# Kernel optimization log

Hardware: AMD Instinct MI355X
Metric: run time of the kernel (lower is better)

Reference implementation:

```python
import jax, jax.numpy as jnp
import numpy as np

N, D, IN_DIM, H, L = 20000, 32, 3, 64, 3


def _lstm_agg(h_nodes, nbr_sorted, W_ih, W_hh, b_ih, b_hh):
    """Batched LSTM over each node's (sorted) neighbor sequence; returns final hidden state h_T."""
    n = h_nodes.shape[0]
    hidden = W_hh.shape[1]

    def step(carry, idx):
        h, c = carry
        x = h_nodes[idx]                                     # [N, in_d] irregular gather
        gates = x @ W_ih.T + h @ W_hh.T + b_ih + b_hh        # [N, 4H], torch gate order i,f,g,o
        i_g, f_g, g_g, o_g = jnp.split(gates, 4, axis=-1)
        c = jax.nn.sigmoid(f_g) * c + jax.nn.sigmoid(i_g) * jnp.tanh(g_g)
        h = jax.nn.sigmoid(o_g) * jnp.tanh(c)
        return (h, c), None

    init = (jnp.zeros((n, hidden), h_nodes.dtype), jnp.zeros((n, hidden), h_nodes.dtype))
    (h_T, _), _ = jax.lax.scan(step, init, nbr_sorted.T)      # scan over D neighbor slots
    return h_T


def _layer(h, nbr_sorted, W_ih, W_hh, b_ih, b_hh, Wl, bl):
    agg = _lstm_agg(h, nbr_sorted, W_ih, W_hh, b_ih, b_hh)    # [N, H]
    comb = jnp.concatenate([h, agg], axis=-1)                 # [N, in_d + H]
    return jax.nn.relu(comb @ Wl.T + bl)


def _forward(node_features, nbr, params, W_out, b_out):
    nbr_sorted = jnp.sort(nbr, axis=1)   # permutation-invariant ordering (Eq. 9)
    h = node_features
    for p in params:
        h = _layer(h, nbr_sorted, *p)
    return (h @ W_out.T + b_out).squeeze(-1)   # [N] per-node log-likelihood scores


def setup_inputs():
    key = jax.random.key(0)
    ks = jax.random.split(key, 40)
    inp = {}
    inp["node_features"] = jax.random.normal(ks[0], (N, IN_DIM), jnp.float32)
    inp["nbr"] = jax.random.randint(ks[1], (N, D), 0, N, jnp.int32)
    k = 2
    s = 1.0 / np.sqrt(H)
    for l in range(L):
        in_d = IN_DIM if l == 0 else H
        inp[f"W_ih{l}"] = (jax.random.normal(ks[k], (4 * H, in_d)) * (1.0 / np.sqrt(in_d))).astype(jnp.float32); k += 1
        inp[f"W_hh{l}"] = (jax.random.normal(ks[k], (4 * H, H)) * s).astype(jnp.float32); k += 1
        inp[f"b_ih{l}"] = (jax.random.normal(ks[k], (4 * H,)) * s).astype(jnp.float32); k += 1
        inp[f"b_hh{l}"] = (jax.random.normal(ks[k], (4 * H,)) * s).astype(jnp.float32); k += 1
        inp[f"Wl{l}"] = (jax.random.normal(ks[k], (H, in_d + H)) * (1.0 / np.sqrt(in_d + H))).astype(jnp.float32); k += 1
        inp[f"bl{l}"] = (jax.random.normal(ks[k], (H,)) * s).astype(jnp.float32); k += 1
    inp["W_out"] = (jax.random.normal(ks[k], (1, H)) * s).astype(jnp.float32); k += 1
    inp["b_out"] = jnp.zeros((1,), jnp.float32)
    return inp


def reference(node_features, nbr, W_ih0, W_hh0, b_ih0, b_hh0, Wl0, bl0, W_ih1, W_hh1, b_ih1, b_hh1, Wl1, bl1, W_ih2, W_hh2, b_ih2, b_hh2, Wl2, bl2, W_out, b_out):
    params = [
        (W_ih0, W_hh0, b_ih0, b_hh0, Wl0, bl0),
        (W_ih1, W_hh1, b_ih1, b_hh1, Wl1, bl1),
        (W_ih2, W_hh2, b_ih2, b_hh2, Wl2, bl2),
    ]
    return _forward(node_features, nbr, params, W_out, b_out)
```

## Files before the change

kernel.cpp:

```cpp
#include <hip/hip_runtime.h>
#include <hip/hip_bf16.h>

#define NN 20000
#define NG 1250
#define LOG2E 1.44269504088896f
#define TWOLOG2E 2.88539008177793f

typedef __attribute__((ext_vector_type(8))) short short8;
typedef __attribute__((ext_vector_type(4))) float floatx4;

__device__ __forceinline__ floatx4 MF(short8 a, short8 b, floatx4 c) {
    return __builtin_amdgcn_mfma_f32_16x16x32_bf16(a, b, c, 0, 0, 0);
}
__device__ __forceinline__ float ex2(float x) { return __builtin_amdgcn_exp2f(x); }
__device__ __forceinline__ float rcp(float x) { return __builtin_amdgcn_rcpf(x); }
__device__ __forceinline__ float clamp30(float x) {
    return __builtin_fminf(__builtin_fmaxf(x, -30.f), 30.f);
}
__device__ __forceinline__ unsigned short bf16r(float x) {
    return __builtin_bit_cast(unsigned short, __float2bfloat16(x));
}
__device__ __forceinline__ void lds_barrier() {
    asm volatile("s_waitcnt lgkmcnt(0)\n\ts_barrier" ::: "memory");
}
__device__ __forceinline__ int rowswz(int L) {
    return L ^ (((L >> 4) & 1) << 1) ^ ((L >> 3) & 1);
}

#define PREP_TOT (40960 + 49152 + 12288 + 12288 + 768 + 640000)
__global__ void prep_kernel(const float* __restrict__ x, const int* __restrict__ nbr,
    const float* __restrict__ Wih0, const float* __restrict__ Whh0,
    const float* __restrict__ bih0, const float* __restrict__ bhh0, const float* __restrict__ Wl0,
    const float* __restrict__ Wih1, const float* __restrict__ Whh1,
    const float* __restrict__ bih1, const float* __restrict__ bhh1, const float* __restrict__ Wl1,
    const float* __restrict__ Wih2, const float* __restrict__ Whh2,
    const float* __restrict__ bih2, const float* __restrict__ bhh2, const float* __restrict__ Wl2,
    unsigned short* __restrict__ Wih_p, unsigned short* __restrict__ Whh_p,
    unsigned short* __restrict__ Wlx_p, unsigned short* __restrict__ Wlh_p,
    float* __restrict__ bsum, unsigned short* __restrict__ x32, int* __restrict__ nbrT)
{
    int tid = blockIdx.x * 256 + threadIdx.x;
    if (tid < NN) {
        int v[32];
        const int4* src = (const int4*)(nbr + tid * 32);
        #pragma unroll
        for (int i = 0; i < 8; i++) {
            int4 t = src[i];
            v[4*i] = t.x; v[4*i+1] = t.y; v[4*i+2] = t.z; v[4*i+3] = t.w;
        }
        #pragma unroll
        for (int k = 2; k <= 32; k <<= 1)
            #pragma unroll
            for (int j = k >> 1; j > 0; j >>= 1)
                #pragma unroll
                for (int i = 0; i < 32; i++) {
                    int ixj = i ^ j;
                    if (ixj > i) {
                        bool up = (i & k) == 0;
                        int a = v[i], b = v[ixj];
                        bool sw = up ? (a > b) : (a < b);
                        if (sw) { v[i] = b; v[ixj] = a; }
                    }
                }
        int g = tid >> 4, m = tid & 15;
        int base = g * 512 + m;
        #pragma unroll
        for (int t = 0; t < 32; t++) nbrT[base + t * 16] = v[t];
    }
    for (int i = blockIdx.x * 256 + threadIdx.x; i < PREP_TOT; i += gridDim.x * 256) {
        int j = i;
        if (j < 40960) {
            if (j < 8192) {
                int jL = j & 7, lane = (j >> 3) & 63, t = (j >> 9) & 7, w = (j >> 12) & 1;
                int col = 64*(t>>1) + 32*w + 16*(t&1) + (lane & 15);
                int k   = (lane >> 4)*8 + jL;
                float sc = ((t>>1) == 2) ? TWOLOG2E : LOG2E;
                Wih_p[j] = bf16r((k < 3) ? Wih0[col*3 + k] * sc : 0.f);
            } else {
                int jj = j - 8192; int l = (jj >> 14) + 1; jj &= 16383;
                int jL = jj & 7, lane = (jj >> 3) & 63, kc = (jj >> 9) & 1;
                int t = (jj >> 10) & 7, w = (jj >> 13) & 1;
                int col = 64*(t>>1) + 32*w + 16*(t&1) + (lane & 15);
                int k   = kc*32 + (lane >> 4)*8 + jL;
                const float* W = (l == 1) ? Wih1 : Wih2;
                float sc = ((t>>1) == 2) ? TWOLOG2E : LOG2E;
                Wih_p[j] = bf16r(W[col*64 + k] * sc);
            }
            continue;
        }
        j -= 40960;
        if (j < 49152) {
            int l = j >> 14, e = j & 16383;
            int col = e >> 6, k = e & 63;
            const float* W = (l == 0) ? Whh0 : ((l == 1) ? Whh1 : Whh2);
            float sc = (col >= 128 && col < 192) ? TWOLOG2E : LOG2E;
            Whh_p[l*16384 + e] = bf16r(W[col*64 + k] * sc);
            continue;
        }
        j -= 49152;
        if (j < 12288) {
            int l = j >> 12, e = j & 4095;
            if (l == 0) {
                if (e < 2048) {
                    int col = e >> 5, k = e & 31;
                    float v = (k < 3) ? Wl0[col*67 + k] : 0.f;
                    Wlx_p[e] = bf16r(v);
                }
            } else {
                int col = e >> 6, k = e & 63;
                const float* W = (l == 1) ? Wl1 : Wl2;
                Wlx_p[l*4096 + e] = bf16r(W[col*128 + k]);
            }
            continue;
        }
        j -= 12288;
        if (j < 12288) {
            int l = j >> 12, e = j & 4095;
            int col = e >> 6, k = e & 63;
            float v = (l == 0) ? Wl0[col*67 + 3 + k]
                               : ((l == 1) ? Wl1 : Wl2)[col*128 + 64 + k];
            Wlh_p[l*4096 + e] = bf16r(v);
            continue;
        }
        j -= 12288;
        if (j < 768) {
            int l = j >> 8, col = j & 255;
            const float* bi = (l == 0) ? bih0 : ((l == 1) ? bih1 : bih2);
            const float* bh = (l == 0) ? bhh0 : ((l == 1) ? bhh1 : bhh2);
            float sc = (col >= 128 && col < 192) ? TWOLOG2E : LOG2E;
            bsum[l*256 + col] = (bi[col] + bh[col]) * sc;
            continue;
        }
        j -= 768;
        {
            int n = j >> 5, k = j & 31;
            x32[j] = bf16r((k < 3) ? x[n*3 + k] : 0.f);
        }
    }
}

template<int XKC, int LASTL>
__global__ __launch_bounds__(128, 2)
void lstm_mfma_kernel(const unsigned short* __restrict__ xsrc,
                      const int* __restrict__ nbrT,
                      const unsigned short* __restrict__ Wih,
                      const unsigned short* __restrict__ Whh,
                      const float* __restrict__ bsum,
                      const unsigned short* __restrict__ Wlx,
                      const unsigned short* __restrict__ Wlh,
                      const float* __restrict__ bl,
                      const float* __restrict__ W_out,
                      const float* __restrict__ b_out,
                      void* __restrict__ hout)
{
    __shared__ unsigned short sA[2][1024];
    __shared__ float sRed[4][16];

    const int w    = threadIdx.x >> 6;
    const int lane = threadIdx.x & 63;
    const int q    = lane >> 4;
    const int c    = lane & 15;
    const int XS   = XKC * 32;

    const int g = blockIdx.x;
    const int node0 = g * 16;
    const int* nbg = nbrT + g * 512;

    short8 fWih[8][XKC];
    short8 fWhh[8][2];
    float  biasv[8];
    #pragma unroll
    for (int t = 0; t < 8; t++) {
        int col = 64*(t>>1) + 32*w + 16*(t&1) + c;
        biasv[t] = bsum[col];
        #pragma unroll
        for (int kc = 0; kc < XKC; kc++)
            fWih[t][kc] = *(const short8*)(Wih + ((w*8 + t)*XKC + kc)*512 + lane*8);
        fWhh[t][0] = *(const short8*)(Whh + col*64 + q*8);
        fWhh[t][1] = *(const short8*)(Whh + col*64 + 32 + q*8);
    }
    floatx4 zeroC = {0.f, 0.f, 0.f, 0.f};

    int idx = nbg[c];
    short8 xg[XKC];
    #pragma unroll
    for (int kc = 0; kc < XKC; kc++)
        xg[kc] = *(const short8*)(xsrc + (long)idx * XS + kc*32 + q*8);

    floatx4 acc[8];
    #pragma unroll
    for (int t = 0; t < 8; t++) {
        acc[t] = MF(xg[0], fWih[t][0], zeroC);
        if (XKC == 2) acc[t] = MF(xg[1], fWih[t][1], acc[t]);
    }
    idx = nbg[16 + c];
    #pragma unroll
    for (int kc = 0; kc < XKC; kc++)
        xg[kc] = *(const short8*)(xsrc + (long)idx * XS + kc*32 + q*8);
    int idx2 = nbg[32 + c];

    float cst[8] = {0.f,0.f,0.f,0.f,0.f,0.f,0.f,0.f};
    short8 hA[2];

    #pragma unroll 1
    for (int t = 0; t < 32; t++) {
        if (t > 0) {
            #pragma unroll
            for (int t8 = 0; t8 < 8; t8++) {
                acc[t8] = MF(hA[0], fWhh[t8][0], acc[t8]);
                acc[t8] = MF(hA[1], fWhh[t8][1], acc[t8]);
            }
        }
        unsigned short* buf = sA[(t + 1) & 1];
        #pragma unroll
        for (int s = 0; s < 2; s++) {
            const int u = 32*w + 16*s + c;
            #pragma unroll
            for (int r = 0; r < 4; r++) {
                float gi = clamp30(acc[0 + s][r] + biasv[0 + s]);
                float gf = clamp30(acc[2 + s][r] + biasv[2 + s]);
                float gg = clamp30(acc[4 + s][r] + biasv[4 + s]);
                float go = clamp30(acc[6 + s][r] + biasv[6 + s]);
                float ei = ex2(-gi), ef = ex2(-gf), eg = ex2(-gg), eo = ex2(-go);
                float pf = 1.f + ef;
                float p  = (1.f + ei) * (1.f + eg);
                float num = fmaf(cst[4*s + r], p, (1.f - eg) * pf);
                float cm  = num * rcp(p * pf);
                cst[4*s + r] = cm;
                float ec = ex2(-clamp30(TWOLOG2E * cm));
                float h  = (1.f - ec) * rcp((1.f + eo) * (1.f + ec));
                int row = 4*q + r + 16*(u >> 3);
                buf[rowswz(row)*8 + (u & 7)] = bf16r(h);
            }
        }
        if (t < 31) {
            #pragma unroll
            for (int t8 = 0; t8 < 8; t8++) {
                acc[t8] = MF(xg[0], fWih[t8][0], zeroC);
                if (XKC == 2) acc[t8] = MF(xg[1], fWih[t8][1], acc[t8]);
            }
            if (t < 30) {
                #pragma unroll
                for (int kc = 0; kc < XKC; kc++)
                    xg[kc] = *(const short8*)(xsrc + (long)idx2 * XS + kc*32 + q*8);
                int tn = (t + 3 < 32) ? t + 3 : 31;
                idx2 = nbg[tn*16 + c];
            }
        }
        lds_barrier();
        const unsigned short* rd = sA[(t + 1) & 1];
        hA[0] = *(const short8*)(rd + rowswz(lane)*8);
        hA[1] = *(const short8*)(rd + 512 + rowswz(lane)*8);
    }

    short8 hin[XKC];
    #pragma unroll
    for (int kc = 0; kc < XKC; kc++)
        hin[kc] = *(const short8*)(xsrc + (long)(node0 + c) * XS + kc*32 + q*8);

    #pragma unroll
    for (int s = 0; s < 2; s++) {
        int col = 32*w + 16*s + c;
        float blv = bl[col];
        floatx4 a; a[0] = blv; a[1] = blv; a[2] = blv; a[3] = blv;
        short8 fx0 = *(const short8*)(Wlx + col*XS + q*8);
        a = MF(hin[0], fx0, a);
        if (XKC == 2) {
            short8 fx1 = *(const short8*)(Wlx + col*XS + 32 + q*8);
            a = MF(hin[1], fx1, a);
        }
        short8 fh0 = *(const short8*)(Wlh + col*64 + q*8);
        short8 fh1 = *(const short8*)(Wlh + col*64 + 32 + q*8);
        a = MF(hA[0], fh0, a);
        a = MF(hA[1], fh1, a);

        if (!LASTL) {
            #pragma unroll
            for (int r = 0; r < 4; r++)
                ((unsigned short*)hout)[(node0 + 4*q + r) * 64 + col] = bf16r(fmaxf(a[r], 0.f));
        } else {
            float wo = W_out[col];
            float pr[4];
            #pragma unroll
            for (int r = 0; r < 4; r++) pr[r] = fmaxf(a[r], 0.f) * wo;
            #pragma unroll
            for (int d = 1; d < 16; d <<= 1) {
                #pragma unroll
                for (int r = 0; r < 4; r++) pr[r] += __shfl_xor(pr[r], d);
            }
            if (c == 0) {
                #pragma unroll
                for (int r = 0; r < 4; r++) sRed[2*w + s][4*q + r] = pr[r];
            }
        }
    }
    if (LASTL) {
        lds_barrier();
        if (w == 0 && lane < 16)
            ((float*)hout)[node0 + lane] =
                sRed[0][lane] + sRed[1][lane] + sRed[2][lane] + sRed[3][lane] + b_out[0];
    }
}

extern "C" void kernel_launch(void* const* d_in, const int* in_sizes, int n_in,
                              void* d_out, int out_size, void* d_ws, size_t ws_size,
                              hipStream_t stream) {
    (void)in_sizes; (void)n_in; (void)out_size; (void)ws_size;
    const float* node_features = (const float*)d_in[0];
    const int*   nbr           = (const int*)d_in[1];
    const float* Wih[3] = {(const float*)d_in[2],  (const float*)d_in[8],  (const float*)d_in[14]};
    const float* Whh[3] = {(const float*)d_in[3],  (const float*)d_in[9],  (const float*)d_in[15]};
    const float* bih[3] = {(const float*)d_in[4],  (const float*)d_in[10], (const float*)d_in[16]};
    const float* bhh[3] = {(const float*)d_in[5],  (const float*)d_in[11], (const float*)d_in[17]};
    const float* Wl[3]  = {(const float*)d_in[6],  (const float*)d_in[12], (const float*)d_in[18]};
    const float* bl[3]  = {(const float*)d_in[7],  (const float*)d_in[13], (const float*)d_in[19]};
    const float* W_out  = (const float*)d_in[20];
    const float* b_out  = (const float*)d_in[21];

    char* ws = (char*)d_ws;
    int*            nbrT  = (int*)ws;
    unsigned short* x32   = (unsigned short*)(ws + 2560000);
    unsigned short* hb1   = (unsigned short*)(ws + 3840000);
    unsigned short* hb2   = (unsigned short*)(ws + 6400000);
    unsigned short* Wih_p = (unsigned short*)(ws + 8960000);
    unsigned short* Whh_p = (unsigned short*)(ws + 9041920);
    unsigned short* Wlx_p = (unsigned short*)(ws + 9140224);
    unsigned short* Wlh_p = (unsigned short*)(ws + 9164800);
    float*          bsum  = (float*)(ws + 9189376);

    prep_kernel<<<1024, 256, 0, stream>>>(node_features, nbr,
        Wih[0], Whh[0], bih[0], bhh[0], Wl[0],
        Wih[1], Whh[1], bih[1], bhh[1], Wl[1],
        Wih[2], Whh[2], bih[2], bhh[2], Wl[2],
        Wih_p, Whh_p, Wlx_p, Wlh_p, bsum, x32, nbrT);

    lstm_mfma_kernel<1, 0><<<NG, 128, 0, stream>>>(x32, nbrT,
        Wih_p,          Whh_p,         bsum,       Wlx_p,        Wlh_p,        bl[0],
        nullptr, nullptr, hb1);
    lstm_mfma_kernel<2, 0><<<NG, 128, 0, stream>>>(hb1, nbrT,
        Wih_p + 8192,   Whh_p + 16384, bsum + 256, Wlx_p + 4096, Wlh_p + 4096, bl[1],
        nullptr, nullptr, hb2);
    lstm_mfma_kernel<2, 1><<<NG, 128, 0, stream>>>(hb2, nbrT,
        Wih_p + 24576,  Whh_p + 32768, bsum + 512, Wlx_p + 8192, Wlh_p + 8192, bl[2],
        W_out, b_out, (float*)d_out);
}
```

Before: 349.9 us.

## Give each wavefront a whole 16-node group, staging weights in LDS and dropping barriers

Before, two waves split the 256 gate columns of one 16-node group and had to meet at a block barrier every timestep to exchange hidden states. Now each wave owns all 256 columns of its own group, and a 256-thread block holds four such groups. The input-to-hidden weights and the second half of the hidden-to-hidden weights are loaded into shared memory once per block, and each step uses only a per-wave LDS wait. The host-side weight prep packs both weight matrices into MFMA fragment order to match. In exchange there are more registers per wave (16 accumulators and 16 state values), more LDS traffic each step, and four times fewer blocks.

```diff
diff --git a/kernel.cpp b/kernel.cpp
--- a/kernel.cpp
+++ b/kernel.cpp
@@ -20,8 +20,8 @@
 __device__ __forceinline__ unsigned short bf16r(float x) {
     return __builtin_bit_cast(unsigned short, __float2bfloat16(x));
 }
-__device__ __forceinline__ void lds_barrier() {
-    asm volatile("s_waitcnt lgkmcnt(0)\n\ts_barrier" ::: "memory");
+__device__ __forceinline__ void lds_wait() {
+    asm volatile("s_waitcnt lgkmcnt(0)" ::: "memory");
 }
 __device__ __forceinline__ int rowswz(int L) {
     return L ^ (((L >> 4) & 1) << 1) ^ ((L >> 3) & 1);
@@ -71,19 +71,21 @@
         int j = i;
         if (j < 40960) {
             if (j < 8192) {
-                int jL = j & 7, lane = (j >> 3) & 63, t = (j >> 9) & 7, w = (j >> 12) & 1;
-                int col = 64*(t>>1) + 32*w + 16*(t&1) + (lane & 15);
-                int k   = (lane >> 4)*8 + jL;
-                float sc = ((t>>1) == 2) ? TWOLOG2E : LOG2E;
+                int ti = (j >> 9) & 15, lane = (j >> 3) & 63, jj = j & 7;
+                int col = 16*ti + (lane & 15);
+                int k   = (lane >> 4)*8 + jj;
+                float sc = (ti >= 8 && ti < 12) ? TWOLOG2E : LOG2E;
                 Wih_p[j] = bf16r((k < 3) ? Wih0[col*3 + k] * sc : 0.f);
             } else {
-                int jj = j - 8192; int l = (jj >> 14) + 1; jj &= 16383;
-                int jL = jj & 7, lane = (jj >> 3) & 63, kc = (jj >> 9) & 1;
-                int t = (jj >> 10) & 7, w = (jj >> 13) & 1;
-                int col = 64*(t>>1) + 32*w + 16*(t&1) + (lane & 15);
-                int k   = kc*32 + (lane >> 4)*8 + jL;
+                int jp = j - 8192;
+                int l  = 1 + (jp >> 14);
+                int e  = jp & 16383;
+                int kc = e >> 13, rem = e & 8191;
+                int ti = rem >> 9, lane = (rem >> 3) & 63, jj = rem & 7;
+                int col = 16*ti + (lane & 15);
+                int k   = kc*32 + (lane >> 4)*8 + jj;
                 const float* W = (l == 1) ? Wih1 : Wih2;
-                float sc = ((t>>1) == 2) ? TWOLOG2E : LOG2E;
+                float sc = (ti >= 8 && ti < 12) ? TWOLOG2E : LOG2E;
                 Wih_p[j] = bf16r(W[col*64 + k] * sc);
             }
             continue;
@@ -91,10 +93,13 @@
         j -= 40960;
         if (j < 49152) {
             int l = j >> 14, e = j & 16383;
-            int col = e >> 6, k = e & 63;
+            int kc = e >> 13, rem = e & 8191;
+            int ti = rem >> 9, lane = (rem >> 3) & 63, jj = rem & 7;
+            int col = 16*ti + (lane & 15);
+            int k   = kc*32 + (lane >> 4)*8 + jj;
             const float* W = (l == 0) ? Whh0 : ((l == 1) ? Whh1 : Whh2);
-            float sc = (col >= 128 && col < 192) ? TWOLOG2E : LOG2E;
-            Whh_p[l*16384 + e] = bf16r(W[col*64 + k] * sc);
+            float sc = (ti >= 8 && ti < 12) ? TWOLOG2E : LOG2E;
+            Whh_p[j] = bf16r(W[col*64 + k] * sc);
             continue;
         }
         j -= 49152;
@@ -140,7 +145,7 @@
 }
 
 template<int XKC, int LASTL>
-__global__ __launch_bounds__(128, 2)
+__global__ __launch_bounds__(256, 2)
 void lstm_mfma_kernel(const unsigned short* __restrict__ xsrc,
                       const int* __restrict__ nbrT,
                       const unsigned short* __restrict__ Wih,
@@ -153,33 +158,35 @@
                       const float* __restrict__ b_out,
                       void* __restrict__ hout)
 {
-    __shared__ unsigned short sA[2][1024];
-    __shared__ float sRed[4][16];
-
-    const int w    = threadIdx.x >> 6;
+    __shared__ unsigned short sWih[XKC * 8192];
+    __shared__ unsigned short sWhh1[8192];
+    __shared__ unsigned short sA[4][1024];
+
+    const int wid  = threadIdx.x >> 6;
     const int lane = threadIdx.x & 63;
     const int q    = lane >> 4;
     const int c    = lane & 15;
     const int XS   = XKC * 32;
 
-    const int g = blockIdx.x;
-    const int node0 = g * 16;
-    const int* nbg = nbrT + g * 512;
-
-    short8 fWih[8][XKC];
-    short8 fWhh[8][2];
-    float  biasv[8];
-    #pragma unroll
-    for (int t = 0; t < 8; t++) {
-        int col = 64*(t>>1) + 32*w + 16*(t&1) + c;
-        biasv[t] = bsum[col];
-        #pragma unroll
-        for (int kc = 0; kc < XKC; kc++)
-            fWih[t][kc] = *(const short8*)(Wih + ((w*8 + t)*XKC + kc)*512 + lane*8);
-        fWhh[t][0] = *(const short8*)(Whh + col*64 + q*8);
-        fWhh[t][1] = *(const short8*)(Whh + col*64 + 32 + q*8);
-    }
-    floatx4 zeroC = {0.f, 0.f, 0.f, 0.f};
+    for (int i = threadIdx.x * 8; i < XKC * 8192; i += 2048)
+        *(short8*)(sWih + i) = *(const short8*)(Wih + i);
+    for (int i = threadIdx.x * 8; i < 8192; i += 2048)
+        *(short8*)(sWhh1 + i) = *(const short8*)(Whh + 8192 + i);
+    __syncthreads();
+
+    const int gid = blockIdx.x * 4 + wid;
+    if (gid >= NG) return;
+    const int node0 = gid * 16;
+    const int* nbg = nbrT + gid * 512;
+    unsigned short* sAw = sA[wid];
+
+    short8 fWhh0[16];
+    float  biasv[16];
+    #pragma unroll
+    for (int ti = 0; ti < 16; ti++) {
+        fWhh0[ti] = *(const short8*)(Whh + ti*512 + lane*8);
+        biasv[ti] = bsum[16*ti + c];
+    }
 
     int idx = nbg[c];
     short8 xg[XKC];
@@ -187,11 +194,13 @@
     for (int kc = 0; kc < XKC; kc++)
         xg[kc] = *(const short8*)(xsrc + (long)idx * XS + kc*32 + q*8);
 
-    floatx4 acc[8];
-    #pragma unroll
-    for (int t = 0; t < 8; t++) {
-        acc[t] = MF(xg[0], fWih[t][0], zeroC);
-        if (XKC == 2) acc[t] = MF(xg[1], fWih[t][1], acc[t]);
+    floatx4 acc[16];
+    const floatx4 zeroC = {0.f, 0.f, 0.f, 0.f};
+    #pragma unroll
+    for (int ti = 0; ti < 16; ti++) {
+        acc[ti] = MF(xg[0], *(const short8*)(sWih + ti*512 + lane*8), zeroC);
+        if (XKC == 2)
+            acc[ti] = MF(xg[1], *(const short8*)(sWih + (16 + ti)*512 + lane*8), acc[ti]);
     }
     idx = nbg[16 + c];
     #pragma unroll
@@ -199,45 +208,47 @@
         xg[kc] = *(const short8*)(xsrc + (long)idx * XS + kc*32 + q*8);
     int idx2 = nbg[32 + c];
 
-    float cst[8] = {0.f,0.f,0.f,0.f,0.f,0.f,0.f,0.f};
+    float cst[16];
+    #pragma unroll
+    for (int i = 0; i < 16; i++) cst[i] = 0.f;
     short8 hA[2];
 
     #pragma unroll 1
     for (int t = 0; t < 32; t++) {
         if (t > 0) {
             #pragma unroll
-            for (int t8 = 0; t8 < 8; t8++) {
-                acc[t8] = MF(hA[0], fWhh[t8][0], acc[t8]);
-                acc[t8] = MF(hA[1], fWhh[t8][1], acc[t8]);
-            }
-        }
-        unsigned short* buf = sA[(t + 1) & 1];
-        #pragma unroll
-        for (int s = 0; s < 2; s++) {
-            const int u = 32*w + 16*s + c;
+            for (int ti = 0; ti < 16; ti++) {
+                acc[ti] = MF(hA[0], fWhh0[ti], acc[ti]);
+                acc[ti] = MF(hA[1], *(const short8*)(sWhh1 + ti*512 + lane*8), acc[ti]);
+            }
+        }
+        #pragma unroll
+        for (int us = 0; us < 4; us++) {
+            const int u = 16*us + c;
             #pragma unroll
             for (int r = 0; r < 4; r++) {
-                float gi = clamp30(acc[0 + s][r] + biasv[0 + s]);
-                float gf = clamp30(acc[2 + s][r] + biasv[2 + s]);
-                float gg = clamp30(acc[4 + s][r] + biasv[4 + s]);
-                float go = clamp30(acc[6 + s][r] + biasv[6 + s]);
+                float gi = clamp30(acc[ 0 + us][r] + biasv[ 0 + us]);
+                float gf = clamp30(acc[ 4 + us][r] + biasv[ 4 + us]);
+                float gg = clamp30(acc[ 8 + us][r] + biasv[ 8 + us]);
+                float go = clamp30(acc[12 + us][r] + biasv[12 + us]);
                 float ei = ex2(-gi), ef = ex2(-gf), eg = ex2(-gg), eo = ex2(-go);
                 float pf = 1.f + ef;
                 float p  = (1.f + ei) * (1.f + eg);
-                float num = fmaf(cst[4*s + r], p, (1.f - eg) * pf);
+                float num = fmaf(cst[us*4 + r], p, (1.f - eg) * pf);
                 float cm  = num * rcp(p * pf);
-                cst[4*s + r] = cm;
+                cst[us*4 + r] = cm;
                 float ec = ex2(-clamp30(TWOLOG2E * cm));
                 float h  = (1.f - ec) * rcp((1.f + eo) * (1.f + ec));
                 int row = 4*q + r + 16*(u >> 3);
-                buf[rowswz(row)*8 + (u & 7)] = bf16r(h);
+                sAw[rowswz(row)*8 + (u & 7)] = bf16r(h);
             }
         }
         if (t < 31) {
             #pragma unroll
-            for (int t8 = 0; t8 < 8; t8++) {
-                acc[t8] = MF(xg[0], fWih[t8][0], zeroC);
-                if (XKC == 2) acc[t8] = MF(xg[1], fWih[t8][1], acc[t8]);
+            for (int ti = 0; ti < 16; ti++) {
+                acc[ti] = MF(xg[0], *(const short8*)(sWih + ti*512 + lane*8), zeroC);
+                if (XKC == 2)
+                    acc[ti] = MF(xg[1], *(const short8*)(sWih + (16 + ti)*512 + lane*8), acc[ti]);
             }
             if (t < 30) {
                 #pragma unroll
@@ -247,10 +258,9 @@
                 idx2 = nbg[tn*16 + c];
             }
         }
-        lds_barrier();
-        const unsigned short* rd = sA[(t + 1) & 1];
-        hA[0] = *(const short8*)(rd + rowswz(lane)*8);
-        hA[1] = *(const short8*)(rd + 512 + rowswz(lane)*8);
+        lds_wait();
+        hA[0] = *(const short8*)(sAw + rowswz(lane)*8);
+        hA[1] = *(const short8*)(sAw + 512 + rowswz(lane)*8);
     }
 
     short8 hin[XKC];
@@ -258,47 +268,47 @@
     for (int kc = 0; kc < XKC; kc++)
         hin[kc] = *(const short8*)(xsrc + (long)(node0 + c) * XS + kc*32 + q*8);
 
-    #pragma unroll
-    for (int s = 0; s < 2; s++) {
-        int col = 32*w + 16*s + c;
+    floatx4 av[4];
+    #pragma unroll
+    for (int s = 0; s < 4; s++) {
+        int col = 16*s + c;
         float blv = bl[col];
         floatx4 a; a[0] = blv; a[1] = blv; a[2] = blv; a[3] = blv;
-        short8 fx0 = *(const short8*)(Wlx + col*XS + q*8);
-        a = MF(hin[0], fx0, a);
-        if (XKC == 2) {
-            short8 fx1 = *(const short8*)(Wlx + col*XS + 32 + q*8);
-            a = MF(hin[1], fx1, a);
-        }
-        short8 fh0 = *(const short8*)(Wlh + col*64 + q*8);
-        short8 fh1 = *(const short8*)(Wlh + col*64 + 32 + q*8);
-        a = MF(hA[0], fh0, a);
-        a = MF(hA[1], fh1, a);
-
-        if (!LASTL) {
+        a = MF(hin[0], *(const short8*)(Wlx + col*XS + q*8), a);
+        if (XKC == 2)
+            a = MF(hin[1], *(const short8*)(Wlx + col*XS + 32 + q*8), a);
+        a = MF(hA[0], *(const short8*)(Wlh + col*64 + q*8), a);
+        a = MF(hA[1], *(const short8*)(Wlh + col*64 + 32 + q*8), a);
+        av[s] = a;
+    }
+
+    if (!LASTL) {
+        unsigned short* ho = (unsigned short*)hout;
+        #pragma unroll
+        for (int s = 0; s < 4; s++)
             #pragma unroll
             for (int r = 0; r < 4; r++)
-                ((unsigned short*)hout)[(node0 + 4*q + r) * 64 + col] = bf16r(fmaxf(a[r], 0.f));
-        } else {
-            float wo = W_out[col];
-            float pr[4];
-            #pragma unroll
-            for (int r = 0; r < 4; r++) pr[r] = fmaxf(a[r], 0.f) * wo;
-            #pragma unroll
-            for (int d = 1; d < 16; d <<= 1) {
-                #pragma unroll
-                for (int r = 0; r < 4; r++) pr[r] += __shfl_xor(pr[r], d);
-            }
-            if (c == 0) {
-                #pragma unroll
-                for (int r = 0; r < 4; r++) sRed[2*w + s][4*q + r] = pr[r];
-            }
-        }
-    }
-    if (LASTL) {
-        lds_barrier();
-        if (w == 0 && lane < 16)
-            ((float*)hout)[node0 + lane] =
-                sRed[0][lane] + sRed[1][lane] + sRed[2][lane] + sRed[3][lane] + b_out[0];
+                ho[(node0 + 4*q + r) * 64 + 16*s + c] = bf16r(fmaxf(av[s][r], 0.f));
+    } else {
+        float p[4];
+        #pragma unroll
+        for (int r = 0; r < 4; r++) p[r] = 0.f;
+        #pragma unroll
+        for (int s = 0; s < 4; s++) {
+            float wo = W_out[16*s + c];
+            #pragma unroll
+            for (int r = 0; r < 4; r++) p[r] = fmaf(fmaxf(av[s][r], 0.f), wo, p[r]);
+        }
+        #pragma unroll
+        for (int d = 1; d < 16; d <<= 1)
+            #pragma unroll
+            for (int r = 0; r < 4; r++) p[r] += __shfl_xor(p[r], d);
+        if (c == 0) {
+            float bo = b_out[0];
+            #pragma unroll
+            for (int r = 0; r < 4; r++)
+                ((float*)hout)[node0 + 4*q + r] = p[r] + bo;
+        }
     }
 }
 
@@ -334,13 +344,15 @@
         Wih[2], Whh[2], bih[2], bhh[2], Wl[2],
         Wih_p, Whh_p, Wlx_p, Wlh_p, bsum, x32, nbrT);
 
-    lstm_mfma_kernel<1, 0><<<NG, 128, 0, stream>>>(x32, nbrT,
+    const int GRID = (NG + 3) / 4;
+
+    lstm_mfma_kernel<1, 0><<<GRID, 256, 0, stream>>>(x32, nbrT,
         Wih_p,          Whh_p,         bsum,       Wlx_p,        Wlh_p,        bl[0],
         nullptr, nullptr, hb1);
-    lstm_mfma_kernel<2, 0><<<NG, 128, 0, stream>>>(hb1, nbrT,
+    lstm_mfma_kernel<2, 0><<<GRID, 256, 0, stream>>>(hb1, nbrT,
         Wih_p + 8192,   Whh_p + 16384, bsum + 256, Wlx_p + 4096, Wlh_p + 4096, bl[1],
         nullptr, nullptr, hb2);
-    lstm_mfma_kernel<2, 1><<<NG, 128, 0, stream>>>(hb2, nbrT,
+    lstm_mfma_kernel<2, 1><<<GRID, 256, 0, stream>>>(hb2, nbrT,
         Wih_p + 24576,  Whh_p + 32768, bsum + 512, Wlx_p + 8192, Wlh_p + 8192, bl[2],
         W_out, b_out, (float*)d_out);
 }
```

Measured after the change: 428.7 us. 1.23x slower.
